# Optimization experiments

Measured on AMD Instinct MI355X. Metric: run time of the kernel, lower is better.

Reference implementation:

```python
import jax, jax.numpy as jnp
import numpy as np
import math

BSZ, H, P, L = 8, 512, 256, 4096
DT_MIN, DT_MAX = 1e-3, 1e-1


def setup_inputs() -> dict:
    key = jax.random.key(0)
    ks = jax.random.split(key, 7)
    input_sequence = jax.random.normal(ks[0], (BSZ, 1, H, 1, L), dtype=jnp.float32)
    # HiPPO-like init: negative real parts, spread imaginary parts
    Lambda_re = -(0.1 + jax.random.uniform(ks[1], (P,), dtype=jnp.float32))  # in (-1.1, -0.1)
    Lambda_im = jax.random.normal(ks[2], (P,), dtype=jnp.float32) * math.pi
    B = jax.random.normal(ks[3], (P, H, 2), dtype=jnp.float32) / math.sqrt(H)
    C = jax.random.normal(ks[4], (H, P, 2), dtype=jnp.float32) * (0.5 ** 0.5)
    D = jax.random.normal(ks[5], (H,), dtype=jnp.float32)
    u = jax.random.uniform(ks[6], (P, 1), dtype=jnp.float32)
    log_step = math.log(DT_MIN) + u * (math.log(DT_MAX) - math.log(DT_MIN))
    return {"input_sequence": input_sequence, "Lambda_re": Lambda_re,
            "Lambda_im": Lambda_im, "B": B, "C": C, "D": D, "log_step": log_step}


def _binary_operator(q_i, q_j):
    A_i, b_i = q_i
    A_j, b_j = q_j
    return (A_j * A_i, A_j * b_i + b_j)


def reference(input_sequence, Lambda_re, Lambda_im, B, C, D, log_step):
    # conj_sym=True, clip_eigs=False, activation='gelu'
    Lambda = Lambda_re + 1j * Lambda_im                       # (P,) complex
    B_tilde = B[..., 0] + 1j * B[..., 1]                      # (P,H)
    C_tilde = C[..., 0] + 1j * C[..., 1]                      # (H,P)
    step = jnp.exp(log_step[:, 0])                            # (P,)
    # ZOH discretization
    Lambda_bar = jnp.exp(Lambda * step)                       # (P,)
    B_bar = ((Lambda_bar - 1.0) / Lambda)[:, None] * B_tilde  # (P,H)
    # (bsz,1,H,1,L) -> (bsz,L,H)
    u = input_sequence[:, 0, :, 0].transpose(0, 2, 1)
    Bu = jnp.einsum('ph,blh->blp', B_bar, u.astype(B_bar.dtype))  # (bsz,L,P) complex
    Lambda_elems = jnp.broadcast_to(Lambda_bar, Bu.shape)
    _, xs = jax.lax.associative_scan(_binary_operator, (Lambda_elems, Bu), axis=1)
    ys = 2.0 * jnp.einsum('hp,blp->blh', C_tilde, xs).real    # conj_sym output
    ys = ys + u * D                                           # feedthrough
    ys = jax.nn.gelu(ys, approximate=False)
    return ys.transpose(0, 2, 1)[:, None, :, None, :]         # (bsz,1,H,1,L)
```

## Files before the change

### kernel.cpp

```cpp
#include <hip/hip_runtime.h>
#include <math.h>

#define HH 512
#define PP 256
#define LL 4096
#define NB 8
#define BM 128
#define BN 128
#define BK 32
#define KTILES (HH / BK)

typedef __attribute__((ext_vector_type(4))) float f32x4;
typedef __attribute__((ext_vector_type(8))) __bf16 bf16x8;
typedef __attribute__((ext_vector_type(4))) unsigned short us4;
typedef __attribute__((ext_vector_type(8))) unsigned short us8;


__device__ __forceinline__ unsigned short f2bf(float x) {
  unsigned int u = __builtin_bit_cast(unsigned int, x);
  return (unsigned short)((u + 0x7fffu + ((u >> 16) & 1u)) >> 16);
}
__device__ __forceinline__ float bf2f(unsigned short h) {
  unsigned int u = ((unsigned int)h) << 16;
  return __builtin_bit_cast(float, u);
}
__device__ __forceinline__ float gelu_exact(float x) {
  return 0.5f * x * (1.0f + erff(x * 0.70710678118654752f));
}
__device__ __forceinline__ void gl_lds16(const void* g, void* l) {
  __builtin_amdgcn_global_load_lds(
      (const __attribute__((address_space(1))) unsigned int*)g,
      (__attribute__((address_space(3))) unsigned int*)l, 16, 0, 0);
}

__global__ __launch_bounds__(256) void precompute_params(
    const float* __restrict__ Lre, const float* __restrict__ Lim,
    const float* __restrict__ Bmat, const float* __restrict__ Cmat,
    const float* __restrict__ logstep,
    unsigned short* __restrict__ M1, unsigned short* __restrict__ C2,
    float* __restrict__ lam)
{
  const int p = blockIdx.x;
  const int t = threadIdx.x;
  const float re = Lre[p], im = Lim[p];
  const float step = expf(logstep[p]);
  const float er  = expf(re * step);
  const float lbr = er * cosf(im * step);
  const float lbi = er * sinf(im * step);
  if (t == 0) { lam[2*p] = lbr; lam[2*p+1] = lbi; }
  const float den = re*re + im*im;
  const float nr = lbr - 1.0f, ni = lbi;
  const float gr = (nr*re + ni*im) / den;
  const float gi = (ni*re - nr*im) / den;
  for (int h = t; h < HH; h += 256) {
    const float br = Bmat[(p*HH + h)*2 + 0];
    const float bi = Bmat[(p*HH + h)*2 + 1];
    M1[p*HH + h]        = f2bf(gr*br - gi*bi);
    M1[(PP+p)*HH + h]   = f2bf(gr*bi + gi*br);
    const float cr = Cmat[(h*PP + p)*2 + 0];
    const float ci = Cmat[(h*PP + p)*2 + 1];
    C2[h*(2*PP) + p]      = f2bf( 2.0f * cr);
    C2[h*(2*PP) + PP + p] = f2bf(-2.0f * ci);
  }
}

template<bool SRCF32, bool EPI>
__global__ __launch_bounds__(256, 4) void s5_gemm_fused(
    const unsigned short* __restrict__ A,
    const void* __restrict__ Bsrc,
    void* __restrict__ Cout,
    const float* __restrict__ Dv,
    const float* __restrict__ Ug)
{
  const int nbx = LL / BN;
  const int nby = HH / BM;
  const int nwg = nbx * nby * NB;
  const int hw  = blockIdx.x + nbx * (blockIdx.y + nby * blockIdx.z);
  const int bid = (hw & 7) * (nwg >> 3) + (hw >> 3);
  const int bx = bid % nbx;
  const int by = (bid / nbx) % nby;
  const int b  = bid / (nbx * nby);

  const int n0 = bx * BN;
  const int m0 = by * BM;
  const int tid  = threadIdx.x;
  const int lane = tid & 63;
  const int w    = tid >> 6;
  const int lr = lane & 15, lg = lane >> 4;
  const int wm = (w >> 1) * 64, wn = (w & 1) * 64;

  __shared__ unsigned short As[2][BM * BK];
  __shared__ unsigned short Bs[2][BN * BK];

  f32x4 acc[4][4];
#pragma unroll
  for (int i = 0; i < 4; ++i)
#pragma unroll
    for (int j = 0; j < 4; ++j) acc[i][j] = f32x4{0.0f, 0.0f, 0.0f, 0.0f};

  const int swz = (lg ^ ((lr >> 2) & 3)) * 8;

  const int nq = tid & 31;
  const int ko = tid >> 5;

  const float*          BsF = (const float*)Bsrc          + (size_t)b * HH * LL;
  const unsigned short* BsH = (const unsigned short*)Bsrc + (size_t)b * HH * LL;

  f32x4 bv[4];
  us4   bh[4];

#define STAGE_A(k0, sel)                                                       \
  {                                                                            \
    _Pragma("unroll")                                                          \
    for (int i = 0; i < 2; ++i) {                                              \
      const int c   = i * 256 + tid;                                           \
      const int row = c >> 2;                                                  \
      const int ks  = (c & 3) ^ ((c >> 4) & 3);                                \
      gl_lds16(A + (size_t)(m0 + row) * HH + (k0) + ks * 8, &As[sel][c * 8]);  \
    }                                                                          \
  }

#define B_LOAD(k0)                                                             \
  {                                                                            \
    _Pragma("unroll")                                                          \
    for (int r = 0; r < 4; ++r) {                                              \
      if (SRCF32)                                                              \
        bv[r] = *(const f32x4*)(BsF + (size_t)((k0) + ko * 4 + r) * LL + n0 + nq * 4); \
      else                                                                     \
        bh[r] = *(const us4*)(BsH + (size_t)((k0) + ko * 4 + r) * LL + n0 + nq * 4);   \
    }                                                                          \
  }

#define B_WRITE(sel)                                                           \
  {                                                                            \
    _Pragma("unroll")                                                          \
    for (int j = 0; j < 4; ++j) {                                              \
      const int n2 = nq * 4 + j;                                               \
      us4 wv;                                                                  \
      _Pragma("unroll")                                                        \
      for (int r = 0; r < 4; ++r)                                              \
        wv[r] = SRCF32 ? f2bf(bv[r][j]) : bh[r][j];                            \
      const int slot = (ko >> 1) ^ ((n2 >> 2) & 3);                            \
      *(us4*)&Bs[sel][n2 * BK + slot * 8 + (ko & 1) * 4] = wv;                 \
    }                                                                          \
  }

  B_LOAD(0);
  STAGE_A(0, 0);
  B_WRITE(0);
  __syncthreads();

  for (int t = 0; t < KTILES; ++t) {
    const int cur = t & 1;
    const bool more = (t + 1 < KTILES);
    if (more) {
      B_LOAD((t + 1) * BK);
      if (cur) STAGE_A((t + 1) * BK, 0) else STAGE_A((t + 1) * BK, 1);
      asm volatile("s_waitcnt vmcnt(6)" ::: "memory");
    } else {
      asm volatile("s_waitcnt vmcnt(0)" ::: "memory");
    }
    __builtin_amdgcn_sched_barrier(0);
    __builtin_amdgcn_s_barrier();
    __builtin_amdgcn_sched_barrier(0);

    bf16x8 aF[4], bF[4];
#pragma unroll
    for (int f = 0; f < 4; ++f) {
      aF[f] = *(const bf16x8*)&As[cur][(wm + f * 16 + lr) * BK + swz];
      bF[f] = *(const bf16x8*)&Bs[cur][(wn + f * 16 + lr) * BK + swz];
    }
#pragma unroll
    for (int fm = 0; fm < 4; ++fm)
#pragma unroll
      for (int fn = 0; fn < 4; ++fn)
        acc[fm][fn] = __builtin_amdgcn_mfma_f32_16x16x32_bf16(
            aF[fm], bF[fn], acc[fm][fn], 0, 0, 0);
    if (more) {
      if (cur) B_WRITE(0) else B_WRITE(1);
    }
    asm volatile("s_waitcnt lgkmcnt(0)" ::: "memory");
    __builtin_amdgcn_sched_barrier(0);
    __builtin_amdgcn_s_barrier();
    __builtin_amdgcn_sched_barrier(0);
  }
#undef STAGE_A
#undef B_LOAD
#undef B_WRITE

  if (!EPI) {
    unsigned short* C = (unsigned short*)Cout + (size_t)b * HH * LL;
#pragma unroll
    for (int fm = 0; fm < 4; ++fm)
#pragma unroll
      for (int r = 0; r < 4; ++r) {
        const int row = m0 + wm + fm*16 + lg*4 + r;
#pragma unroll
        for (int fn = 0; fn < 4; ++fn) {
          const int col = n0 + wn + fn*16 + lr;
          C[(size_t)row * LL + col] = f2bf(acc[fm][fn][r]);
        }
      }
  } else {
    float* C = (float*)Cout + (size_t)b * HH * LL;
    const float* Ub = Ug + (size_t)b * HH * LL;
#pragma unroll
    for (int fm = 0; fm < 4; ++fm)
#pragma unroll
      for (int r = 0; r < 4; ++r) {
        const int row = m0 + wm + fm*16 + lg*4 + r;
        const float dv = Dv[row];
#pragma unroll
        for (int fn = 0; fn < 4; ++fn) {
          const int col = n0 + wn + fn*16 + lr;
          const float y = fmaf(dv, Ub[(size_t)row * LL + col], acc[fm][fn][r]);
          C[(size_t)row * LL + col] = gelu_exact(y);
        }
      }
  }
}

__global__ __launch_bounds__(256) void s5_scan(
    unsigned short* __restrict__ Bu, const float* __restrict__ lam)
{
  const int p = blockIdx.x;
  const int b = blockIdx.y;
  const int t = threadIdx.x;
  unsigned short* rowr = Bu + ((size_t)b*2*PP + p)      * LL;
  unsigned short* rowi = Bu + ((size_t)b*2*PP + PP + p) * LL;

  const float lre = lam[2*p], lim = lam[2*p+1];

  float br[16], bi[16];
  {
    us8 v0 = *(const us8*)&rowr[t*16];
    us8 v1 = *(const us8*)&rowr[t*16 + 8];
    us8 w0 = *(const us8*)&rowi[t*16];
    us8 w1 = *(const us8*)&rowi[t*16 + 8];
#pragma unroll
    for (int j = 0; j < 8; ++j) {
      br[j] = bf2f(v0[j]); br[8+j] = bf2f(v1[j]);
      bi[j] = bf2f(w0[j]); bi[8+j] = bf2f(w1[j]);
    }
  }

  float xr = 0.0f, xi = 0.0f;
#pragma unroll
  for (int j = 0; j < 16; ++j) {
    const float nr = fmaf(lre, xr, fmaf(-lim, xi, br[j]));
    const float ni = fmaf(lre, xi, fmaf( lim, xr, bi[j]));
    xr = nr; xi = ni;
  }

  float mre = lre, mim = lim;
#pragma unroll
  for (int s = 0; s < 4; ++s) {
    const float nr2 = mre*mre - mim*mim;
    mim = 2.0f*mre*mim; mre = nr2;
  }

  __shared__ float sre[256], sim[256];
  float tre = xr, tim = xi;
  sre[t] = tre; sim[t] = tim;
  __syncthreads();
  for (int o = 1; o < 256; o <<= 1) {
    float pr = 0.0f, pi = 0.0f;
    if (t >= o) { pr = sre[t-o]; pi = sim[t-o]; }
    __syncthreads();
    if (t >= o) {
      tre += mre*pr - mim*pi;
      tim += mre*pi + mim*pr;
      sre[t] = tre; sim[t] = tim;
    }
    __syncthreads();
    const float nr2 = mre*mre - mim*mim;
    mim = 2.0f*mre*mim; mre = nr2;
  }

  float cr = 0.0f, ci = 0.0f;
  if (t > 0) { cr = sre[t-1]; ci = sim[t-1]; }

  xr = cr; xi = ci;
  us8 o0, o1, o2, o3;
#pragma unroll
  for (int j = 0; j < 16; ++j) {
    const float nr = fmaf(lre, xr, fmaf(-lim, xi, br[j]));
    const float ni = fmaf(lre, xi, fmaf( lim, xr, bi[j]));
    xr = nr; xi = ni;
    if (j < 8) { o0[j] = f2bf(xr); o2[j] = f2bf(xi); }
    else       { o1[j-8] = f2bf(xr); o3[j-8] = f2bf(xi); }
  }
  *(us8*)&rowr[t*16]     = o0;
  *(us8*)&rowr[t*16 + 8] = o1;
  *(us8*)&rowi[t*16]     = o2;
  *(us8*)&rowi[t*16 + 8] = o3;
}

extern "C" void kernel_launch(void* const* d_in, const int* in_sizes, int n_in,
                              void* d_out, int out_size, void* d_ws, size_t ws_size,
                              hipStream_t stream) {
  (void)in_sizes; (void)n_in; (void)out_size; (void)ws_size;
  const float* in_seq = (const float*)d_in[0];
  const float* Lre    = (const float*)d_in[1];
  const float* Lim    = (const float*)d_in[2];
  const float* Bm     = (const float*)d_in[3];
  const float* Cm     = (const float*)d_in[4];
  const float* Dv     = (const float*)d_in[5];
  const float* ls     = (const float*)d_in[6];
  float* out = (float*)d_out;

  char* ws = (char*)d_ws;
  unsigned short* M1  = (unsigned short*)(ws);
  unsigned short* C2  = (unsigned short*)(ws + (512u << 10));
  float*          lam = (float*)(ws + (1u << 20));
  unsigned short* Bu  = (unsigned short*)(ws + (2u << 20));

  precompute_params<<<dim3(PP), dim3(256), 0, stream>>>(Lre, Lim, Bm, Cm, ls, M1, C2, lam);

  dim3 gg(LL/BN, HH/BM, NB);
  s5_gemm_fused<true, false><<<gg, dim3(256), 0, stream>>>(M1, in_seq, Bu, nullptr, nullptr);

  s5_scan<<<dim3(PP, NB), dim3(256), 0, stream>>>(Bu, lam);

  s5_gemm_fused<false, true><<<gg, dim3(256), 0, stream>>>(C2, Bu, out, Dv, in_seq);
}
```

Measured before the change: 103.9 us.

## Use wave-shuffle scan in s5_scan and stage GEMM bf16 output through LDS

The cross-thread prefix scan in s5_scan now uses wavefront __shfl_up rounds plus a small cross-wave combine through four shared slots, replacing a Hillis-Steele scan that needed two block barriers per step over 8 steps. It rebuilds the carry-in by multiplying lambda powers according to the lane bits. Separately, the bf16 GEMM epilogue writes the tile into the reused LDS buffer and then stores it with coalesced 16-byte writes instead of scattered 2-byte stores. The LDS buffers are merged into one aligned array so the epilogue can reuse it.

```diff
diff --git a/kernel.cpp b/kernel.cpp
--- a/kernel.cpp
+++ b/kernel.cpp
@@ -89,8 +89,11 @@
   const int lr = lane & 15, lg = lane >> 4;
   const int wm = (w >> 1) * 64, wn = (w & 1) * 64;
 
-  __shared__ unsigned short As[2][BM * BK];
-  __shared__ unsigned short Bs[2][BN * BK];
+  __shared__ __align__(16) unsigned short LB[4 * BM * BK];
+  unsigned short* const As0 = LB;
+  unsigned short* const Bs0 = LB + 2 * BM * BK;
+#define ASEL(s) (As0 + (s) * BM * BK)
+#define BSEL(s) (Bs0 + (s) * BN * BK)
 
   f32x4 acc[4][4];
 #pragma unroll
@@ -116,7 +119,7 @@
       const int c   = i * 256 + tid;                                           \
       const int row = c >> 2;                                                  \
       const int ks  = (c & 3) ^ ((c >> 4) & 3);                                \
-      gl_lds16(A + (size_t)(m0 + row) * HH + (k0) + ks * 8, &As[sel][c * 8]);  \
+      gl_lds16(A + (size_t)(m0 + row) * HH + (k0) + ks * 8, &ASEL(sel)[c * 8]);\
     }                                                                          \
   }
 
@@ -141,7 +144,7 @@
       for (int r = 0; r < 4; ++r)                                              \
         wv[r] = SRCF32 ? f2bf(bv[r][j]) : bh[r][j];                            \
       const int slot = (ko >> 1) ^ ((n2 >> 2) & 3);                            \
-      *(us4*)&Bs[sel][n2 * BK + slot * 8 + (ko & 1) * 4] = wv;                 \
+      *(us4*)&BSEL(sel)[n2 * BK + slot * 8 + (ko & 1) * 4] = wv;               \
     }                                                                          \
   }
 
@@ -167,8 +170,8 @@
     bf16x8 aF[4], bF[4];
 #pragma unroll
     for (int f = 0; f < 4; ++f) {
-      aF[f] = *(const bf16x8*)&As[cur][(wm + f * 16 + lr) * BK + swz];
-      bF[f] = *(const bf16x8*)&Bs[cur][(wn + f * 16 + lr) * BK + swz];
+      aF[f] = *(const bf16x8*)&ASEL(cur)[(wm + f * 16 + lr) * BK + swz];
+      bF[f] = *(const bf16x8*)&BSEL(cur)[(wn + f * 16 + lr) * BK + swz];
     }
 #pragma unroll
     for (int fm = 0; fm < 4; ++fm)
@@ -189,18 +192,27 @@
 #undef B_WRITE
 
   if (!EPI) {
-    unsigned short* C = (unsigned short*)Cout + (size_t)b * HH * LL;
 #pragma unroll
     for (int fm = 0; fm < 4; ++fm)
 #pragma unroll
       for (int r = 0; r < 4; ++r) {
-        const int row = m0 + wm + fm*16 + lg*4 + r;
+        const int row = wm + fm * 16 + lg * 4 + r;
 #pragma unroll
         for (int fn = 0; fn < 4; ++fn) {
-          const int col = n0 + wn + fn*16 + lr;
-          C[(size_t)row * LL + col] = f2bf(acc[fm][fn][r]);
+          const int col = wn + fn * 16 + lr;
+          LB[row * 128 + col] = f2bf(acc[fm][fn][r]);
         }
       }
+    __syncthreads();
+    unsigned short* C = (unsigned short*)Cout + (size_t)b * HH * LL;
+#pragma unroll
+    for (int pass = 0; pass < 8; ++pass) {
+      const int chunk = pass * 256 + tid;
+      const int row = chunk >> 4;
+      const int c8  = chunk & 15;
+      us8 v = *(const us8*)&LB[row * 128 + c8 * 8];
+      *(us8*)(C + (size_t)(m0 + row) * LL + n0 + c8 * 8) = v;
+    }
   } else {
     float* C = (float*)Cout + (size_t)b * HH * LL;
     const float* Ub = Ug + (size_t)b * HH * LL;
@@ -218,6 +230,8 @@
         }
       }
   }
+#undef ASEL
+#undef BSEL
 }
 
 __global__ __launch_bounds__(256) void s5_scan(
@@ -226,6 +240,8 @@
   const int p = blockIdx.x;
   const int b = blockIdx.y;
   const int t = threadIdx.x;
+  const int lane = t & 63;
+  const int w    = t >> 6;
   unsigned short* rowr = Bu + ((size_t)b*2*PP + p)      * LL;
   unsigned short* rowi = Bu + ((size_t)b*2*PP + PP + p) * LL;
 
@@ -255,30 +271,53 @@
   float mre = lre, mim = lim;
 #pragma unroll
   for (int s = 0; s < 4; ++s) {
-    const float nr2 = mre*mre - mim*mim;
-    mim = 2.0f*mre*mim; mre = nr2;
-  }
-
-  __shared__ float sre[256], sim[256];
-  float tre = xr, tim = xi;
-  sre[t] = tre; sim[t] = tim;
+    const float n2 = mre*mre - mim*mim;
+    mim = 2.0f*mre*mim; mre = n2;
+  }
+
+  float Sr = xr, Si = xi;
+  float pwr[6], pwi[6];
+#pragma unroll
+  for (int rnd = 0; rnd < 6; ++rnd) {
+    pwr[rnd] = mre; pwi[rnd] = mim;
+    const int off = 1 << rnd;
+    const float vr = __shfl_up(Sr, off);
+    const float vi = __shfl_up(Si, off);
+    if (lane >= off) {
+      Sr = fmaf(mre, vr, fmaf(-mim, vi, Sr));
+      Si = fmaf(mre, vi, fmaf( mim, vr, Si));
+    }
+    const float n2 = mre*mre - mim*mim;
+    mim = 2.0f*mre*mim; mre = n2;
+  }
+
+  __shared__ float Twr[4], Twi[4];
+  if (lane == 63) { Twr[w] = Sr; Twi[w] = Si; }
   __syncthreads();
-  for (int o = 1; o < 256; o <<= 1) {
-    float pr = 0.0f, pi = 0.0f;
-    if (t >= o) { pr = sre[t-o]; pi = sim[t-o]; }
-    __syncthreads();
-    if (t >= o) {
-      tre += mre*pr - mim*pi;
-      tim += mre*pi + mim*pr;
-      sre[t] = tre; sim[t] = tim;
-    }
-    __syncthreads();
-    const float nr2 = mre*mre - mim*mim;
-    mim = 2.0f*mre*mim; mre = nr2;
-  }
-
-  float cr = 0.0f, ci = 0.0f;
-  if (t > 0) { cr = sre[t-1]; ci = sim[t-1]; }
+
+  float cwr = 0.0f, cwi = 0.0f;
+  for (int v = 0; v < w; ++v) {
+    const float nr = fmaf(mre, cwr, fmaf(-mim, cwi, Twr[v]));
+    const float ni = fmaf(mre, cwi, fmaf( mim, cwr, Twi[v]));
+    cwr = nr; cwi = ni;
+  }
+
+  float Er = __shfl_up(Sr, 1);
+  float Ei = __shfl_up(Si, 1);
+  if (lane == 0) { Er = 0.0f; Ei = 0.0f; }
+
+  float plr = 1.0f, pli = 0.0f;
+#pragma unroll
+  for (int rnd = 0; rnd < 6; ++rnd) {
+    if ((lane >> rnd) & 1) {
+      const float nr = plr*pwr[rnd] - pli*pwi[rnd];
+      const float ni = plr*pwi[rnd] + pli*pwr[rnd];
+      plr = nr; pli = ni;
+    }
+  }
+
+  const float cr = Er + plr*cwr - pli*cwi;
+  const float ci = Ei + plr*cwi + pli*cwr;
 
   xr = cr; xi = ci;
   us8 o0, o1, o2, o3;
```

Measured after the change: 103.7 us, median of 2. Within noise of the previous version (-0.2%).
